# Optimization experiments

Hardware: AMD Instinct MI355X
Metric: run time of the kernel (lower is better)

Reference implementation:

```python
import math
import jax, jax.numpy as jnp
import numpy as np

B, S, D, L = 8, 4096, 1024, 16

def setup_inputs() -> dict:
    key = jax.random.key(0)
    k1, k2, k3 = jax.random.split(key, 3)
    memory = jax.random.normal(k1, (B, S, D), dtype=jnp.float32)
    summarizer = jax.random.normal(k2, (L, D), dtype=jnp.float32) * 0.02
    w_proj = jax.random.normal(k3, (1, L), dtype=jnp.float32) * (1.0 / math.sqrt(L))
    return {"memory": memory, "summarizer": summarizer, "w_proj": w_proj}

def reference(memory, summarizer, w_proj):
    # scores: [B, L, S] = summarizer @ memory^T / sqrt(D)
    d = summarizer.shape[-1]
    scores = jnp.einsum('ld,bsd->bls', summarizer, memory) / jnp.sqrt(jnp.asarray(d, memory.dtype))
    p_attn = jax.nn.softmax(scores, axis=-1)            # softmax over sequence S
    ctx = jnp.einsum('bls,bsd->bld', p_attn, memory)    # [B, L, D]
    # nn.Linear(L, 1, bias=False) applied to ctx.transpose(-1,-2): [B, D, L] @ W^T -> [B, D, 1]
    out = jnp.einsum('bld,l->bd', ctx, w_proj[0])       # [B, D]
    return out[:, None, :]                              # [B, 1, D] after final transpose
```

## Files before the change

### kernel.cpp

```cpp
#include <hip/hip_runtime.h>
#include <hip/hip_bf16.h>

#define BB 8
#define SS 4096
#define DD 1024
#define LL 16

typedef __attribute__((ext_vector_type(8))) short short8;
typedef __attribute__((ext_vector_type(4))) float fl4;

static __device__ __forceinline__ short f2bf(float f) {
    unsigned u = __float_as_uint(f);
    u += 0x7FFFu + ((u >> 16) & 1u);
    return (short)(u >> 16);
}

__global__ __launch_bounds__(256) void k_prep(const float* __restrict__ summ,
                                              short* __restrict__ summb,
                                              float* __restrict__ Z,
                                              float* __restrict__ out) {
    int i = blockIdx.x * 256 + threadIdx.x;
    if (i < LL * DD) summb[i] = f2bf(summ[i]);
    if (i < BB * LL) Z[i] = 0.f;
    if (i < BB * DD) out[i] = 0.f;
}

__global__ __launch_bounds__(256, 4) void k_scores(const float* __restrict__ mem,
                                                   const short* __restrict__ summb,
                                                   float* __restrict__ e,
                                                   float* __restrict__ Z) {
    __shared__ float red[2][64 * 4];
    int widx = threadIdx.x >> 6;
    int tp   = widx >> 1;
    int h    = widx & 1;
    int tile = blockIdx.x * 2 + tp;
    int lane = threadIdx.x & 63;
    int b  = tile >> 8;
    int s0 = (tile & 255) << 4;
    int o  = lane & 15;
    int qd = lane >> 4;
    int kb = h << 9;

    const short* arow = summb + o * DD + kb + qd * 8;
    const float* mrow = mem + ((size_t)b * SS + s0 + o) * DD + kb + qd * 8;

    fl4 acc = {0.f, 0.f, 0.f, 0.f};
    fl4 p0 = *(const fl4*)(mrow);
    fl4 p1 = *(const fl4*)(mrow + 4);
    #pragma unroll
    for (int i = 0; i < 16; ++i) {
        fl4 n0, n1;
        if (i < 15) {
            n0 = *(const fl4*)(mrow + (i + 1) * 32);
            n1 = *(const fl4*)(mrow + (i + 1) * 32 + 4);
        }
        short8 a = *(const short8*)(arow + i * 32);
        short8 bb;
        bb[0] = f2bf(p0[0]); bb[1] = f2bf(p0[1]);
        bb[2] = f2bf(p0[2]); bb[3] = f2bf(p0[3]);
        bb[4] = f2bf(p1[0]); bb[5] = f2bf(p1[1]);
        bb[6] = f2bf(p1[2]); bb[7] = f2bf(p1[3]);
        acc = __builtin_amdgcn_mfma_f32_16x16x32_bf16(a, bb, acc, 0, 0, 0);
        p0 = n0; p1 = n1;
    }

    if (h == 1) *(fl4*)&red[tp][lane * 4] = acc;
    __syncthreads();
    if (h == 0) {
        fl4 other = *(const fl4*)&red[tp][lane * 4];
        acc += other;

        const float scale = 0.03125f;
        fl4 ev;
        #pragma unroll
        for (int r = 0; r < 4; ++r) ev[r] = __expf(acc[r] * scale);
        *(fl4*)&e[((size_t)b * SS + s0 + o) * LL + qd * 4] = ev;

        fl4 zs = ev;
        #pragma unroll
        for (int r = 0; r < 4; ++r) {
            float v = zs[r];
            v += __shfl_xor(v, 1, 64);
            v += __shfl_xor(v, 2, 64);
            v += __shfl_xor(v, 4, 64);
            v += __shfl_xor(v, 8, 64);
            zs[r] = v;
        }
        if (o == 0) {
            #pragma unroll
            for (int r = 0; r < 4; ++r) atomicAdd(&Z[b * LL + qd * 4 + r], zs[r]);
        }
    }
}

__global__ __launch_bounds__(256, 4) void k_ctx(const float* __restrict__ mem,
                                                const float* __restrict__ e,
                                                const float* __restrict__ Z,
                                                const float* __restrict__ w,
                                                float* __restrict__ out) {
    int blk = blockIdx.x;
    int b  = blk >> 7;
    int s0 = (blk & 127) << 5;
    int t = threadIdx.x;

    __shared__ float coef[LL];
    __shared__ float qs[32];
    if (t < LL) coef[t] = w[t] / Z[b * LL + t];
    if (t < 32) {
        const float* ep = e + ((size_t)b * SS + s0 + t) * LL;
        float qv = 0.f;
        #pragma unroll
        for (int l = 0; l < LL; ++l) qv += coef[l] * ep[l];
        qs[t] = qv;
    }
    __syncthreads();

    const float* mb = mem + ((size_t)b * SS + s0) * DD + t * 4;
    fl4 acc = {0.f, 0.f, 0.f, 0.f};
    fl4 c = *(const fl4*)(mb);
    #pragma unroll
    for (int i = 0; i < 32; ++i) {
        fl4 n;
        if (i < 31) n = *(const fl4*)(mb + (size_t)(i + 1) * DD);
        acc += qs[i] * c;
        c = n;
    }
    float* op = out + (size_t)b * DD + t * 4;
    atomicAdd(op + 0, acc[0]);
    atomicAdd(op + 1, acc[1]);
    atomicAdd(op + 2, acc[2]);
    atomicAdd(op + 3, acc[3]);
}

extern "C" void kernel_launch(void* const* d_in, const int* in_sizes, int n_in,
                              void* d_out, int out_size, void* d_ws, size_t ws_size,
                              hipStream_t stream) {
    const float* mem  = (const float*)d_in[0];
    const float* summ = (const float*)d_in[1];
    const float* w    = (const float*)d_in[2];
    float* out = (float*)d_out;

    char* ws = (char*)d_ws;
    short* summb = (short*)ws;
    float* Z     = (float*)(ws + 64 * 1024);
    float* e     = (float*)(ws + 68 * 1024);

    k_prep<<<64, 256, 0, stream>>>(summ, summb, Z, out);
    k_scores<<<1024, 256, 0, stream>>>(mem, summb, e, Z);
    k_ctx<<<1024, 256, 0, stream>>>(mem, e, Z, w, out);
}
```

Before: 254.6 us.

## Stage score tiles via global-to-LDS DMA and drop the prep kernel

The scores kernel now runs one 64-thread wave per 16-row tile and streams memory rows into LDS with global_load_lds, padded to avoid bank conflicts, instead of splitting K across two waves and reducing. The prep kernel is removed: the summarizer is converted to bf16 inline, output zeroing moves into the scores kernel, and Z atomics become per-tile partials that the ctx kernel sums. The ctx kernel processes 64 rows per block with batched loads to raise memory-level parallelism and halve the output atomics. In exchange, summarizer conversion is repeated in every tile, and each ctx block re-reduces 256 partials. The DMA loads are also serialized with waitcnt and not double-buffered.

New measurement: 221.8 us. -12.9%, faster.

```diff
diff --git a/kernel.cpp b/kernel.cpp
--- a/kernel.cpp
+++ b/kernel.cpp
@@ -5,6 +5,7 @@
 #define SS 4096
 #define DD 1024
 #define LL 16
+#define RSTRIDE 260
 
 typedef __attribute__((ext_vector_type(8))) short short8;
 typedef __attribute__((ext_vector_type(4))) float fl4;
@@ -15,115 +16,133 @@
     return (short)(u >> 16);
 }
 
-__global__ __launch_bounds__(256) void k_prep(const float* __restrict__ summ,
-                                              short* __restrict__ summb,
-                                              float* __restrict__ Z,
-                                              float* __restrict__ out) {
-    int i = blockIdx.x * 256 + threadIdx.x;
-    if (i < LL * DD) summb[i] = f2bf(summ[i]);
-    if (i < BB * LL) Z[i] = 0.f;
-    if (i < BB * DD) out[i] = 0.f;
+static __device__ __forceinline__ short8 pack8(fl4 a, fl4 b) {
+    short8 r;
+    r[0] = f2bf(a[0]); r[1] = f2bf(a[1]); r[2] = f2bf(a[2]); r[3] = f2bf(a[3]);
+    r[4] = f2bf(b[0]); r[5] = f2bf(b[1]); r[6] = f2bf(b[2]); r[7] = f2bf(b[3]);
+    return r;
 }
 
-__global__ __launch_bounds__(256, 4) void k_scores(const float* __restrict__ mem,
-                                                   const short* __restrict__ summb,
-                                                   float* __restrict__ e,
-                                                   float* __restrict__ Z) {
-    __shared__ float red[2][64 * 4];
-    int widx = threadIdx.x >> 6;
-    int tp   = widx >> 1;
-    int h    = widx & 1;
-    int tile = blockIdx.x * 2 + tp;
-    int lane = threadIdx.x & 63;
+static __device__ __forceinline__ void dma16(const float* g, float* l) {
+    __builtin_amdgcn_global_load_lds(
+        (const __attribute__((address_space(1))) void*)g,
+        (__attribute__((address_space(3))) void*)l, 16, 0, 0);
+}
+
+__global__ __launch_bounds__(64) void k_scores(const float* __restrict__ mem,
+                                               const float* __restrict__ summ,
+                                               float* __restrict__ e,
+                                               float* __restrict__ Zpart,
+                                               float* __restrict__ out) {
+    __shared__ float tl[16 * RSTRIDE];
+    int tile = blockIdx.x;
     int b  = tile >> 8;
     int s0 = (tile & 255) << 4;
+    int lane = threadIdx.x;
     int o  = lane & 15;
     int qd = lane >> 4;
-    int kb = h << 9;
 
-    const short* arow = summb + o * DD + kb + qd * 8;
-    const float* mrow = mem + ((size_t)b * SS + s0 + o) * DD + kb + qd * 8;
+    if (tile < 128) out[tile * 64 + lane] = 0.f;
+
+    const float* grow = mem + ((size_t)b * SS + s0) * DD + lane * 4;
+    const float* arow = summ + o * DD + qd * 8;
 
     fl4 acc = {0.f, 0.f, 0.f, 0.f};
-    fl4 p0 = *(const fl4*)(mrow);
-    fl4 p1 = *(const fl4*)(mrow + 4);
-    #pragma unroll
-    for (int i = 0; i < 16; ++i) {
-        fl4 n0, n1;
-        if (i < 15) {
-            n0 = *(const fl4*)(mrow + (i + 1) * 32);
-            n1 = *(const fl4*)(mrow + (i + 1) * 32 + 4);
+    for (int ks = 0; ks < 4; ++ks) {
+        asm volatile("s_waitcnt lgkmcnt(0)" ::: "memory");
+        const float* gk = grow + ks * 256;
+        #pragma unroll
+        for (int r = 0; r < 16; ++r)
+            dma16(gk + (size_t)r * DD, &tl[r * RSTRIDE]);
+
+        short8 afr[8];
+        #pragma unroll
+        for (int j = 0; j < 8; ++j) {
+            fl4 a0 = *(const fl4*)(arow + ks * 256 + j * 32);
+            fl4 a1 = *(const fl4*)(arow + ks * 256 + j * 32 + 4);
+            afr[j] = pack8(a0, a1);
         }
-        short8 a = *(const short8*)(arow + i * 32);
-        short8 bb;
-        bb[0] = f2bf(p0[0]); bb[1] = f2bf(p0[1]);
-        bb[2] = f2bf(p0[2]); bb[3] = f2bf(p0[3]);
-        bb[4] = f2bf(p1[0]); bb[5] = f2bf(p1[1]);
-        bb[6] = f2bf(p1[2]); bb[7] = f2bf(p1[3]);
-        acc = __builtin_amdgcn_mfma_f32_16x16x32_bf16(a, bb, acc, 0, 0, 0);
-        p0 = n0; p1 = n1;
+
+        asm volatile("s_waitcnt vmcnt(0)" ::: "memory");
+        #pragma unroll
+        for (int j = 0; j < 8; ++j) {
+            fl4 f0 = *(const fl4*)&tl[o * RSTRIDE + j * 32 + qd * 8];
+            fl4 f1 = *(const fl4*)&tl[o * RSTRIDE + j * 32 + qd * 8 + 4];
+            acc = __builtin_amdgcn_mfma_f32_16x16x32_bf16(afr[j], pack8(f0, f1),
+                                                          acc, 0, 0, 0);
+        }
     }
 
-    if (h == 1) *(fl4*)&red[tp][lane * 4] = acc;
-    __syncthreads();
-    if (h == 0) {
-        fl4 other = *(const fl4*)&red[tp][lane * 4];
-        acc += other;
+    const float scale = 0.03125f;
+    fl4 ev;
+    #pragma unroll
+    for (int r = 0; r < 4; ++r) ev[r] = __expf(acc[r] * scale);
+    *(fl4*)&e[((size_t)b * SS + s0 + o) * LL + qd * 4] = ev;
 
-        const float scale = 0.03125f;
-        fl4 ev;
-        #pragma unroll
-        for (int r = 0; r < 4; ++r) ev[r] = __expf(acc[r] * scale);
-        *(fl4*)&e[((size_t)b * SS + s0 + o) * LL + qd * 4] = ev;
-
-        fl4 zs = ev;
-        #pragma unroll
-        for (int r = 0; r < 4; ++r) {
-            float v = zs[r];
-            v += __shfl_xor(v, 1, 64);
-            v += __shfl_xor(v, 2, 64);
-            v += __shfl_xor(v, 4, 64);
-            v += __shfl_xor(v, 8, 64);
-            zs[r] = v;
-        }
-        if (o == 0) {
-            #pragma unroll
-            for (int r = 0; r < 4; ++r) atomicAdd(&Z[b * LL + qd * 4 + r], zs[r]);
-        }
+    fl4 zs = ev;
+    #pragma unroll
+    for (int r = 0; r < 4; ++r) {
+        float v = zs[r];
+        v += __shfl_xor(v, 1, 64);
+        v += __shfl_xor(v, 2, 64);
+        v += __shfl_xor(v, 4, 64);
+        v += __shfl_xor(v, 8, 64);
+        zs[r] = v;
     }
+    if (o == 0) *(fl4*)&Zpart[tile * LL + qd * 4] = zs;
 }
 
-__global__ __launch_bounds__(256, 4) void k_ctx(const float* __restrict__ mem,
-                                                const float* __restrict__ e,
-                                                const float* __restrict__ Z,
-                                                const float* __restrict__ w,
-                                                float* __restrict__ out) {
+__global__ __launch_bounds__(256) void k_ctx(const float* __restrict__ mem,
+                                             const float* __restrict__ e,
+                                             const float* __restrict__ Zpart,
+                                             const float* __restrict__ w,
+                                             float* __restrict__ out) {
     int blk = blockIdx.x;
-    int b  = blk >> 7;
-    int s0 = (blk & 127) << 5;
+    int b  = blk >> 6;
+    int s0 = (blk & 63) << 6;
     int t = threadIdx.x;
+    __shared__ float zz[16][LL];
+    __shared__ float coef[LL];
+    __shared__ float qs[64];
 
-    __shared__ float coef[LL];
-    __shared__ float qs[32];
-    if (t < LL) coef[t] = w[t] / Z[b * LL + t];
-    if (t < 32) {
-        const float* ep = e + ((size_t)b * SS + s0 + t) * LL;
+    {
+        int l = t & 15, g = t >> 4;
+        float zsum = 0.f;
+        #pragma unroll
+        for (int j = 0; j < 16; ++j)
+            zsum += Zpart[(size_t)(b * 256 + g * 16 + j) * LL + l];
+        zz[g][l] = zsum;
+    }
+    __syncthreads();
+    if (t < LL) {
+        float Zt = 0.f;
+        #pragma unroll
+        for (int g = 0; g < 16; ++g) Zt += zz[g][t];
+        coef[t] = w[t] / Zt;
+    }
+    __syncthreads();
+    if (t < 64) {
+        const fl4* ep = (const fl4*)(e + ((size_t)b * SS + s0 + t) * LL);
+        fl4 e0 = ep[0], e1 = ep[1], e2 = ep[2], e3 = ep[3];
         float qv = 0.f;
         #pragma unroll
-        for (int l = 0; l < LL; ++l) qv += coef[l] * ep[l];
+        for (int r = 0; r < 4; ++r)
+            qv += coef[r] * e0[r] + coef[4 + r] * e1[r] +
+                  coef[8 + r] * e2[r] + coef[12 + r] * e3[r];
         qs[t] = qv;
     }
     __syncthreads();
 
     const float* mb = mem + ((size_t)b * SS + s0) * DD + t * 4;
     fl4 acc = {0.f, 0.f, 0.f, 0.f};
-    fl4 c = *(const fl4*)(mb);
-    #pragma unroll
-    for (int i = 0; i < 32; ++i) {
-        fl4 n;
-        if (i < 31) n = *(const fl4*)(mb + (size_t)(i + 1) * DD);
-        acc += qs[i] * c;
-        c = n;
+    for (int g = 0; g < 4; ++g) {
+        fl4 v[16];
+        #pragma unroll
+        for (int j = 0; j < 16; ++j)
+            v[j] = *(const fl4*)(mb + (size_t)(g * 16 + j) * DD);
+        #pragma unroll
+        for (int j = 0; j < 16; ++j)
+            acc += qs[g * 16 + j] * v[j];
     }
     float* op = out + (size_t)b * DD + t * 4;
     atomicAdd(op + 0, acc[0]);
@@ -141,11 +160,9 @@
     float* out = (float*)d_out;
 
     char* ws = (char*)d_ws;
-    short* summb = (short*)ws;
-    float* Z     = (float*)(ws + 64 * 1024);
-    float* e     = (float*)(ws + 68 * 1024);
+    float* Zpart = (float*)ws;
+    float* e     = (float*)(ws + 128 * 1024);
 
-    k_prep<<<64, 256, 0, stream>>>(summ, summb, Z, out);
-    k_scores<<<1024, 256, 0, stream>>>(mem, summb, e, Z);
-    k_ctx<<<1024, 256, 0, stream>>>(mem, e, Z, w, out);
+    k_scores<<<BB * SS / 16, 64, 0, stream>>>(mem, summ, e, Zpart, out);
+    k_ctx<<<BB * 64, 256, 0, stream>>>(mem, e, Zpart, w, out);
 }
```
